# Kernel tuning notes

Hardware: AMD Instinct MI355X
Metric: run time of the kernel (lower is better)

## Reference

```python
import jax, jax.numpy as jnp
import numpy as np

N_NODES = 100000
N_EDGES = 1600000
IN_FEATS = 128
HIDDEN = 128
NUM_CLASSES = 4


def setup_inputs() -> dict:
    key = jax.random.key(0)
    ks = jax.random.split(key, 8)
    features = jax.random.normal(ks[0], (N_NODES, IN_FEATS), dtype=jnp.float32)
    src = jax.random.randint(ks[1], (N_EDGES,), 0, N_NODES, dtype=jnp.int64)
    dst = jax.random.randint(ks[2], (N_EDGES,), 0, N_NODES, dtype=jnp.int64)
    s = 1.0 / np.sqrt(IN_FEATS)
    W1 = jax.random.normal(ks[3], (IN_FEATS, HIDDEN), dtype=jnp.float32) * s
    b1 = jnp.zeros((HIDDEN,), dtype=jnp.float32)
    W2 = jax.random.normal(ks[4], (HIDDEN, HIDDEN), dtype=jnp.float32) * s
    b2 = jnp.zeros((HIDDEN,), dtype=jnp.float32)
    Wc = jax.random.normal(ks[5], (HIDDEN, NUM_CLASSES), dtype=jnp.float32) * s
    bc = jnp.zeros((NUM_CLASSES,), dtype=jnp.float32)
    return {"features": features, "src": src, "dst": dst,
            "W1": W1, "b1": b1, "W2": W2, "b2": b2, "Wc": Wc, "bc": bc}


def _graph_conv(x, W, b, src, dst, n_nodes, activation=True):
    # DGL GraphConv, norm='both': D_out^{-1/2} A^T D_in... i.e. symmetric norm.
    ones = jnp.ones((src.shape[0],), dtype=x.dtype)
    deg_out = jnp.clip(jax.ops.segment_sum(ones, src, num_segments=n_nodes), 1.0)
    deg_in = jnp.clip(jax.ops.segment_sum(ones, dst, num_segments=n_nodes), 1.0)
    # scale sources, project (in >= out so matmul first, math-equivalent), gather-scatter
    h = (x * (deg_out ** -0.5)[:, None]) @ W            # [N, out]
    msg = h[src]                                         # [E, out] gather
    agg = jax.ops.segment_sum(msg, dst, num_segments=n_nodes)  # [N, out] scatter-add
    h = agg * (deg_in ** -0.5)[:, None] + b
    return jax.nn.relu(h) if activation else h


def reference(features, src, dst, W1, b1, W2, b2, Wc, bc):
    # eval-mode forward: dropout is identity
    n = features.shape[0]
    h = _graph_conv(features, W1, b1, src, dst, n, activation=True)
    h = _graph_conv(h, W2, b2, src, dst, n, activation=True)
    return h @ Wc + bc  # [N, num_classes] logits
```

## Files before the change

kernel.cpp:

```cpp
#include <hip/hip_runtime.h>
#include <hip/hip_fp16.h>
#include <math.h>

#define N_NODES 100000
#define N_EDGES 1600000
#define F 128
#define NBUK 196
#define BSH 9
#define BSZ 512
#define CAP 10240
#define NPART 784

typedef _Float16 half8 __attribute__((ext_vector_type(8)));
typedef float    f32x4 __attribute__((ext_vector_type(4)));
typedef int      i32x4 __attribute__((ext_vector_type(4)));

__global__ __launch_bounds__(256) void init_pack(int* __restrict__ curD,
                                                 int* __restrict__ curS,
                                                 _Float16* __restrict__ padrow1,
                                                 _Float16* __restrict__ padrow2,
                                                 const float* __restrict__ W1,
                                                 const float* __restrict__ W2,
                                                 _Float16* __restrict__ hi1,
                                                 _Float16* __restrict__ lo1,
                                                 _Float16* __restrict__ hi2,
                                                 _Float16* __restrict__ lo2)
{
    int t = threadIdx.x;
    if (blockIdx.x == 0) {
        if (t < NBUK) { curD[t] = t * CAP; curS[t] = t * CAP; }
        if (t < 16) reinterpret_cast<int4*>(padrow1)[t] = make_int4(0, 0, 0, 0);
        else if (t >= 32 && t < 48) reinterpret_cast<int4*>(padrow2)[t - 32] = make_int4(0, 0, 0, 0);
        return;
    }
    int gidx = (blockIdx.x - 1) * 256 + t;
    const float* W = (gidx < 16384) ? W1 : W2;
    _Float16* hi = (gidx < 16384) ? hi1 : hi2;
    _Float16* lo = (gidx < 16384) ? lo1 : lo2;
    int idx = gidx & 16383;
    int f = idx >> 9, r = idx & 511;
    int l = r >> 3, j = r & 7;
    int kc = f >> 3, ct = f & 7;
    int k = kc * 32 + (l >> 4) * 8 + j;
    int n = ct * 16 + (l & 15);
    float w = W[k * 128 + n];
    _Float16 h = (_Float16)w;
    hi[idx] = h;
    lo[idx] = (_Float16)(w - (float)h);
}

__global__ __launch_bounds__(512) void part_gemm1(const int* __restrict__ src,
                                                  const int* __restrict__ dst,
                                                  int* __restrict__ curD,
                                                  int* __restrict__ curS,
                                                  int* __restrict__ bukD,
                                                  unsigned short* __restrict__ bukS,
                                                  const float* __restrict__ X,
                                                  const _Float16* __restrict__ Whi,
                                                  const _Float16* __restrict__ Wlo,
                                                  _Float16* __restrict__ Y, int N)
{
    __shared__ int hd[NBUK], hs[NBUK], bd[NBUK], bs[NBUK], cd[NBUK], cs[NBUK];
    const int tid = threadIdx.x;

    if (blockIdx.x < NPART) {
        const int chunk = (((N_EDGES + NPART - 1) / NPART) + 3) & ~3;
        const int beg = blockIdx.x * chunk;
        const int end = min(beg + chunk, N_EDGES);
        if (beg >= end) return;
        if (tid < NBUK) { hd[tid] = 0; hs[tid] = 0; cd[tid] = 0; cs[tid] = 0; }
        __syncthreads();
        const int b4 = beg >> 2, e4 = end >> 2;
        const int i0 = b4 + tid;
        const bool v0 = i0 < e4;
        i32x4 d0 = {}, s0 = {};
        if (v0) {
            d0 = reinterpret_cast<const i32x4*>(dst)[i0];
            s0 = reinterpret_cast<const i32x4*>(src)[i0];
            atomicAdd(&hd[d0.x >> BSH], 1); atomicAdd(&hd[d0.y >> BSH], 1);
            atomicAdd(&hd[d0.z >> BSH], 1); atomicAdd(&hd[d0.w >> BSH], 1);
            atomicAdd(&hs[s0.x >> BSH], 1); atomicAdd(&hs[s0.y >> BSH], 1);
            atomicAdd(&hs[s0.z >> BSH], 1); atomicAdd(&hs[s0.w >> BSH], 1);
        }
        __syncthreads();
        if (tid < NBUK) {
            bd[tid] = hd[tid] ? atomicAdd(&curD[tid], hd[tid]) : 0;
            bs[tid] = hs[tid] ? atomicAdd(&curS[tid], hs[tid]) : 0;
        }
        __syncthreads();
        if (v0) {
            int dd[4] = { d0.x, d0.y, d0.z, d0.w };
            int ss[4] = { s0.x, s0.y, s0.z, s0.w };
            #pragma unroll
            for (int j = 0; j < 4; j++) {
                int bin = dd[j] >> BSH;
                int r = atomicAdd(&cd[bin], 1);
                bukD[bd[bin] + r] = ((dd[j] & 511) << 17) | ss[j];
                int bin2 = ss[j] >> BSH;
                int r2 = atomicAdd(&cs[bin2], 1);
                bukS[bs[bin2] + r2] = (unsigned short)(ss[j] & 511);
            }
        }
        return;
    }

    const int l = tid & 63, w = tid >> 6;
    const int quad = l >> 4, m = l & 15;
    const int row0 = (blockIdx.x - NPART) * 256;
    const half8* Bh = reinterpret_cast<const half8*>(Whi);
    const half8* Bl = reinterpret_cast<const half8*>(Wlo);

    f32x4 acc[2][8] = {};

    for (int kc = 0; kc < 4; kc++) {
        half8 ah[2];
        #pragma unroll
        for (int rt = 0; rt < 2; rt++) {
            int grow = row0 + w * 32 + rt * 16 + m;
            float4 xa = make_float4(0.f, 0.f, 0.f, 0.f), xb = xa;
            if (grow < N) {
                const float4* Xp = reinterpret_cast<const float4*>(X) + (size_t)grow * 32 + kc * 8 + quad * 2;
                xa = Xp[0]; xb = Xp[1];
            }
            ah[rt][0] = (_Float16)xa.x; ah[rt][1] = (_Float16)xa.y;
            ah[rt][2] = (_Float16)xa.z; ah[rt][3] = (_Float16)xa.w;
            ah[rt][4] = (_Float16)xb.x; ah[rt][5] = (_Float16)xb.y;
            ah[rt][6] = (_Float16)xb.z; ah[rt][7] = (_Float16)xb.w;
        }
        #pragma unroll
        for (int ct = 0; ct < 8; ct++) {
            int f = kc * 8 + ct;
            half8 bh = Bh[f * 64 + l];
            half8 bl = Bl[f * 64 + l];
            #pragma unroll
            for (int rt = 0; rt < 2; rt++) {
                acc[rt][ct] = __builtin_amdgcn_mfma_f32_16x16x32_f16(ah[rt], bh, acc[rt][ct], 0, 0, 0);
                acc[rt][ct] = __builtin_amdgcn_mfma_f32_16x16x32_f16(ah[rt], bl, acc[rt][ct], 0, 0, 0);
            }
        }
    }

    #pragma unroll
    for (int rt = 0; rt < 2; rt++) {
        #pragma unroll
        for (int r = 0; r < 4; r++) {
            int grow = row0 + w * 32 + rt * 16 + quad * 4 + r;
            if (grow < N) {
                #pragma unroll
                for (int ct = 0; ct < 8; ct++)
                    Y[(size_t)grow * 128 + ct * 16 + m] = (_Float16)(acc[rt][ct][r]);
            }
        }
    }
}

__global__ __launch_bounds__(512) void deg_out(const unsigned short* __restrict__ bukS,
                                               const int* __restrict__ curS,
                                               float* __restrict__ sout)
{
    __shared__ int h[BSZ];
    const int tid = threadIdx.x;
    const int n0 = blockIdx.x << BSH;
    const int lo = blockIdx.x * CAP, hi = curS[blockIdx.x];
    const int cnt = hi - lo;
    h[tid] = 0;
    __syncthreads();
    const uint4* p8 = reinterpret_cast<const uint4*>(bukS + lo);
    const int nv = cnt >> 3;
    for (int j = tid; j < nv; j += 512) {
        uint4 v = p8[j];
        atomicAdd(&h[v.x & 0xFFFF], 1); atomicAdd(&h[v.x >> 16], 1);
        atomicAdd(&h[v.y & 0xFFFF], 1); atomicAdd(&h[v.y >> 16], 1);
        atomicAdd(&h[v.z & 0xFFFF], 1); atomicAdd(&h[v.z >> 16], 1);
        atomicAdd(&h[v.w & 0xFFFF], 1); atomicAdd(&h[v.w >> 16], 1);
    }
    for (int i = lo + (nv << 3) + tid; i < hi; i += 512)
        atomicAdd(&h[bukS[i]], 1);
    __syncthreads();
    int node = n0 + tid;
    if (node < N_NODES) sout[node] = rsqrtf((float)max(h[tid], 1));
}

__global__ __launch_bounds__(512) void csr_wv(const int* __restrict__ bukD,
                                              const int* __restrict__ curD,
                                              const float* __restrict__ sout,
                                              int* __restrict__ row_ptr,
                                              float* __restrict__ sin_,
                                              int* __restrict__ col,
                                              float* __restrict__ wv)
{
    __shared__ int h[BSZ], sc[BSZ], cur[BSZ];
    const int tid = threadIdx.x;
    const int n0 = blockIdx.x << BSH;
    const int lo = blockIdx.x * CAP, hi = curD[blockIdx.x];
    const int cnt = hi - lo;
    h[tid] = 0;
    __syncthreads();
    const i32x4* p4 = reinterpret_cast<const i32x4*>(bukD + lo);
    const int nv = cnt >> 2;
    for (int j = tid; j < nv; j += 512) {
        i32x4 v = p4[j];
        atomicAdd(&h[((unsigned)v.x) >> 17], 1);
        atomicAdd(&h[((unsigned)v.y) >> 17], 1);
        atomicAdd(&h[((unsigned)v.z) >> 17], 1);
        atomicAdd(&h[((unsigned)v.w) >> 17], 1);
    }
    for (int i = lo + (nv << 2) + tid; i < hi; i += 512)
        atomicAdd(&h[((unsigned)bukD[i]) >> 17], 1);
    __syncthreads();
    int own = h[tid];
    int own4 = (own + 3) & ~3;
    sc[tid] = own4;
    __syncthreads();
    for (int off = 1; off < 512; off <<= 1) {
        int u = (tid >= off) ? sc[tid - off] : 0;
        __syncthreads();
        sc[tid] += u;
        __syncthreads();
    }
    int ex = sc[tid] - own4;
    cur[tid] = ex;
    int node = n0 + tid;
    if (node < N_NODES) {
        row_ptr[2 * node]     = lo + ex;
        row_ptr[2 * node + 1] = lo + ex + own4;
        sin_[node] = rsqrtf((float)max(own, 1));
    }
    __syncthreads();
    for (int j = tid; j < nv; j += 512) {
        i32x4 v = p4[j];
        int pv[4] = { v.x, v.y, v.z, v.w };
        #pragma unroll
        for (int q = 0; q < 4; q++) {
            int p = pv[q];
            int s = p & 0x1FFFF;
            int r = atomicAdd(&cur[((unsigned)p) >> 17], 1);
            col[lo + r] = s;
            wv[lo + r]  = sout[s];
        }
    }
    for (int i = lo + (nv << 2) + tid; i < hi; i += 512) {
        int p = bukD[i];
        int s = p & 0x1FFFF;
        int r = atomicAdd(&cur[((unsigned)p) >> 17], 1);
        col[lo + r] = s;
        wv[lo + r]  = sout[s];
    }
    for (int k = own; k < own4; k++) {
        col[lo + ex + k] = N_NODES;
        wv[lo + ex + k]  = 0.f;
    }
}

#define ACCW(vv, ww) \
    a0 = fmaf(ww, (float)vv[0], a0); a1 = fmaf(ww, (float)vv[1], a1); \
    a2 = fmaf(ww, (float)vv[2], a2); a3 = fmaf(ww, (float)vv[3], a3); \
    a4 = fmaf(ww, (float)vv[4], a4); a5 = fmaf(ww, (float)vv[5], a5); \
    a6 = fmaf(ww, (float)vv[6], a6); a7 = fmaf(ww, (float)vv[7], a7);

#define ACCU(vv) \
    a0 += (float)vv[0]; a1 += (float)vv[1]; a2 += (float)vv[2]; a3 += (float)vv[3]; \
    a4 += (float)vv[4]; a5 += (float)vv[5]; a6 += (float)vv[6]; a7 += (float)vv[7];

__global__ __launch_bounds__(256) void gather_gemm2(const _Float16* __restrict__ Hh,
                                                    const int* __restrict__ row_ptr,
                                                    const int* __restrict__ col,
                                                    const float* __restrict__ wv,
                                                    const float* __restrict__ sin_,
                                                    const float* __restrict__ bias,
                                                    const _Float16* __restrict__ Whi,
                                                    const _Float16* __restrict__ Wlo,
                                                    const float* __restrict__ sout,
                                                    _Float16* __restrict__ Y)
{
    __shared__ _Float16 At[16][128];
    const int tid = threadIdx.x;
    const int sub  = tid & 15;
    const int g0   = tid >> 4;
    const int node = blockIdx.x * 16 + g0;
    const int beg = row_ptr[2 * node], end = row_ptr[2 * node + 1];
    const half8* __restrict__ H8 = reinterpret_cast<const half8*>(Hh);

    float a0 = 0.f, a1 = 0.f, a2 = 0.f, a3 = 0.f, a4 = 0.f, a5 = 0.f, a6 = 0.f, a7 = 0.f;
    int i = beg;
    for (; i + 8 <= end; i += 8) {
        int4 ca = *reinterpret_cast<const int4*>(col + i);
        int4 cb = *reinterpret_cast<const int4*>(col + i + 4);
        float4 wa = *reinterpret_cast<const float4*>(wv + i);
        float4 wb = *reinterpret_cast<const float4*>(wv + i + 4);
        half8 v0 = H8[((size_t)ca.x << 4) | sub];
        half8 v1 = H8[((size_t)ca.y << 4) | sub];
        half8 v2 = H8[((size_t)ca.z << 4) | sub];
        half8 v3 = H8[((size_t)ca.w << 4) | sub];
        half8 v4 = H8[((size_t)cb.x << 4) | sub];
        half8 v5 = H8[((size_t)cb.y << 4) | sub];
        half8 v6 = H8[((size_t)cb.z << 4) | sub];
        half8 v7 = H8[((size_t)cb.w << 4) | sub];
        ACCW(v0, wa.x) ACCW(v1, wa.y) ACCW(v2, wa.z) ACCW(v3, wa.w)
        ACCW(v4, wb.x) ACCW(v5, wb.y) ACCW(v6, wb.z) ACCW(v7, wb.w)
    }
    if (i < end) {
        int4 ca = *reinterpret_cast<const int4*>(col + i);
        float4 wa = *reinterpret_cast<const float4*>(wv + i);
        half8 v0 = H8[((size_t)ca.x << 4) | sub];
        half8 v1 = H8[((size_t)ca.y << 4) | sub];
        half8 v2 = H8[((size_t)ca.z << 4) | sub];
        half8 v3 = H8[((size_t)ca.w << 4) | sub];
        ACCW(v0, wa.x) ACCW(v1, wa.y) ACCW(v2, wa.z) ACCW(v3, wa.w)
    }
    {
        float scn = sin_[node];
        const float4* B4 = reinterpret_cast<const float4*>(bias);
        float4 bA = B4[2 * sub], bB = B4[2 * sub + 1];
        half8 o;
        o[0] = (_Float16)fmaxf(fmaf(a0, scn, bA.x), 0.f);
        o[1] = (_Float16)fmaxf(fmaf(a1, scn, bA.y), 0.f);
        o[2] = (_Float16)fmaxf(fmaf(a2, scn, bA.z), 0.f);
        o[3] = (_Float16)fmaxf(fmaf(a3, scn, bA.w), 0.f);
        o[4] = (_Float16)fmaxf(fmaf(a4, scn, bB.x), 0.f);
        o[5] = (_Float16)fmaxf(fmaf(a5, scn, bB.y), 0.f);
        o[6] = (_Float16)fmaxf(fmaf(a6, scn, bB.z), 0.f);
        o[7] = (_Float16)fmaxf(fmaf(a7, scn, bB.w), 0.f);
        int wc = sub ^ (g0 & 7);
        *reinterpret_cast<half8*>(&At[g0][wc * 8]) = o;
    }
    __syncthreads();

    const int l = tid & 63, w = tid >> 6;
    const int quad = l >> 4, m = l & 15;
    const half8* Bh = reinterpret_cast<const half8*>(Whi);
    const half8* Bl = reinterpret_cast<const half8*>(Wlo);

    f32x4 acc0 = {}, acc1 = {};
    #pragma unroll
    for (int kc = 0; kc < 4; kc++) {
        int rc = (kc * 4 + quad) ^ (m & 7);
        half8 a = *reinterpret_cast<const half8*>(&At[m][rc * 8]);
        int f0 = kc * 8 + w * 2;
        half8 bh0 = Bh[f0 * 64 + l];
        half8 bl0 = Bl[f0 * 64 + l];
        half8 bh1 = Bh[(f0 + 1) * 64 + l];
        half8 bl1 = Bl[(f0 + 1) * 64 + l];
        acc0 = __builtin_amdgcn_mfma_f32_16x16x32_f16(a, bh0, acc0, 0, 0, 0);
        acc0 = __builtin_amdgcn_mfma_f32_16x16x32_f16(a, bl0, acc0, 0, 0, 0);
        acc1 = __builtin_amdgcn_mfma_f32_16x16x32_f16(a, bh1, acc1, 0, 0, 0);
        acc1 = __builtin_amdgcn_mfma_f32_16x16x32_f16(a, bl1, acc1, 0, 0, 0);
    }

    const int rbase = blockIdx.x * 16 + quad * 4;
    const int c0 = (w * 2) * 16 + m;
    #pragma unroll
    for (int r = 0; r < 4; r++) {
        int grow = rbase + r;
        float s = sout[grow];
        Y[(size_t)grow * 128 + c0]      = (_Float16)(acc0[r] * s);
        Y[(size_t)grow * 128 + c0 + 16] = (_Float16)(acc1[r] * s);
    }
}

__global__ __launch_bounds__(256) void gather_cls(const _Float16* __restrict__ Hh,
                                                  const int* __restrict__ row_ptr,
                                                  const int* __restrict__ col,
                                                  const float* __restrict__ sin_,
                                                  const float* __restrict__ bias,
                                                  const float* __restrict__ Wc,
                                                  const float* __restrict__ bc,
                                                  float* __restrict__ out, int N)
{
    __shared__ float4 Wcs[128];
    for (int t = threadIdx.x; t < 128; t += 256)
        Wcs[t] = reinterpret_cast<const float4*>(Wc)[t];
    __syncthreads();

    const int sub  = threadIdx.x & 15;
    const int node = blockIdx.x * 16 + (threadIdx.x >> 4);
    if (node >= N) return;
    const int beg = row_ptr[2 * node], end = row_ptr[2 * node + 1];
    const half8* __restrict__ H8 = reinterpret_cast<const half8*>(Hh);

    float a0 = 0.f, a1 = 0.f, a2 = 0.f, a3 = 0.f, a4 = 0.f, a5 = 0.f, a6 = 0.f, a7 = 0.f;
    int i = beg;
    for (; i + 8 <= end; i += 8) {
        int4 ca = *reinterpret_cast<const int4*>(col + i);
        int4 cb = *reinterpret_cast<const int4*>(col + i + 4);
        half8 v0 = H8[((size_t)ca.x << 4) | sub];
        half8 v1 = H8[((size_t)ca.y << 4) | sub];
        half8 v2 = H8[((size_t)ca.z << 4) | sub];
        half8 v3 = H8[((size_t)ca.w << 4) | sub];
        half8 v4 = H8[((size_t)cb.x << 4) | sub];
        half8 v5 = H8[((size_t)cb.y << 4) | sub];
        half8 v6 = H8[((size_t)cb.z << 4) | sub];
        half8 v7 = H8[((size_t)cb.w << 4) | sub];
        ACCU(v0) ACCU(v1) ACCU(v2) ACCU(v3)
        ACCU(v4) ACCU(v5) ACCU(v6) ACCU(v7)
    }
    if (i < end) {
        int4 ca = *reinterpret_cast<const int4*>(col + i);
        half8 v0 = H8[((size_t)ca.x << 4) | sub];
        half8 v1 = H8[((size_t)ca.y << 4) | sub];
        half8 v2 = H8[((size_t)ca.z << 4) | sub];
        half8 v3 = H8[((size_t)ca.w << 4) | sub];
        ACCU(v0) ACCU(v1) ACCU(v2) ACCU(v3)
    }
    float scn = sin_[node];
    const float4* B4 = reinterpret_cast<const float4*>(bias);
    float4 bA = B4[2 * sub], bB = B4[2 * sub + 1];
    float h0 = fmaxf(fmaf(a0, scn, bA.x), 0.f);
    float h1 = fmaxf(fmaf(a1, scn, bA.y), 0.f);
    float h2 = fmaxf(fmaf(a2, scn, bA.z), 0.f);
    float h3 = fmaxf(fmaf(a3, scn, bA.w), 0.f);
    float h4 = fmaxf(fmaf(a4, scn, bB.x), 0.f);
    float h5 = fmaxf(fmaf(a5, scn, bB.y), 0.f);
    float h6 = fmaxf(fmaf(a6, scn, bB.z), 0.f);
    float h7 = fmaxf(fmaf(a7, scn, bB.w), 0.f);

    float lx = 0.f, ly = 0.f, lz = 0.f, lw = 0.f;
    float4 w;
    w = Wcs[sub * 8 + 0]; lx = fmaf(h0, w.x, lx); ly = fmaf(h0, w.y, ly); lz = fmaf(h0, w.z, lz); lw = fmaf(h0, w.w, lw);
    w = Wcs[sub * 8 + 1]; lx = fmaf(h1, w.x, lx); ly = fmaf(h1, w.y, ly); lz = fmaf(h1, w.z, lz); lw = fmaf(h1, w.w, lw);
    w = Wcs[sub * 8 + 2]; lx = fmaf(h2, w.x, lx); ly = fmaf(h2, w.y, ly); lz = fmaf(h2, w.z, lz); lw = fmaf(h2, w.w, lw);
    w = Wcs[sub * 8 + 3]; lx = fmaf(h3, w.x, lx); ly = fmaf(h3, w.y, ly); lz = fmaf(h3, w.z, lz); lw = fmaf(h3, w.w, lw);
    w = Wcs[sub * 8 + 4]; lx = fmaf(h4, w.x, lx); ly = fmaf(h4, w.y, ly); lz = fmaf(h4, w.z, lz); lw = fmaf(h4, w.w, lw);
    w = Wcs[sub * 8 + 5]; lx = fmaf(h5, w.x, lx); ly = fmaf(h5, w.y, ly); lz = fmaf(h5, w.z, lz); lw = fmaf(h5, w.w, lw);
    w = Wcs[sub * 8 + 6]; lx = fmaf(h6, w.x, lx); ly = fmaf(h6, w.y, ly); lz = fmaf(h6, w.z, lz); lw = fmaf(h6, w.w, lw);
    w = Wcs[sub * 8 + 7]; lx = fmaf(h7, w.x, lx); ly = fmaf(h7, w.y, ly); lz = fmaf(h7, w.z, lz); lw = fmaf(h7, w.w, lw);

    #pragma unroll
    for (int m = 1; m < 16; m <<= 1) {
        lx += __shfl_xor(lx, m);
        ly += __shfl_xor(ly, m);
        lz += __shfl_xor(lz, m);
        lw += __shfl_xor(lw, m);
    }
    if (sub == 0) {
        float4 bcv = reinterpret_cast<const float4*>(bc)[0];
        float4 r;
        r.x = lx + bcv.x; r.y = ly + bcv.y; r.z = lz + bcv.z; r.w = lw + bcv.w;
        reinterpret_cast<float4*>(out)[node] = r;
    }
}

extern "C" void kernel_launch(void* const* d_in, const int* in_sizes, int n_in,
                              void* d_out, int out_size, void* d_ws, size_t ws_size,
                              hipStream_t stream)
{
    const float* features = (const float*)d_in[0];
    const int*   src      = (const int*)d_in[1];
    const int*   dst      = (const int*)d_in[2];
    const float* W1       = (const float*)d_in[3];
    const float* b1       = (const float*)d_in[4];
    const float* W2       = (const float*)d_in[5];
    const float* b2       = (const float*)d_in[6];
    const float* Wc       = (const float*)d_in[7];
    const float* bc       = (const float*)d_in[8];
    float* out = (float*)d_out;

    char* ws = (char*)d_ws;
    const size_t MB = 1 << 20;
    int* curD  = (int*)(ws + 0);
    int* curS  = (int*)(ws + 1024);
    _Float16* Whi1 = (_Float16*)(ws + 64 * 1024);
    _Float16* Wlo1 = (_Float16*)(ws + 96 * 1024);
    _Float16* Whi2 = (_Float16*)(ws + 128 * 1024);
    _Float16* Wlo2 = (_Float16*)(ws + 160 * 1024);
    float* sout    = (float*)(ws + 512 * 1024);
    float* sin_    = (float*)(ws + 1 * MB);
    int*   row_ptr = (int*)(ws + 2 * MB);
    int*   col     = (int*)(ws + 3 * MB);
    float* wv      = (float*)(ws + 11 * MB);
    _Float16* hMsg = (_Float16*)(ws + 25 * MB);
    int*   bukD    = (int*)(ws + 52 * MB);
    unsigned short* bukS = (unsigned short*)(ws + 60 * MB);
    _Float16* hA   = (_Float16*)(ws + 52 * MB);

    const int N = N_NODES;
    const int NGB = (N + 15) / 16;

    init_pack<<<129, 256, 0, stream>>>(curD, curS,
                                       hMsg + (size_t)N * F, hA + (size_t)N * F,
                                       W1, W2, Whi1, Wlo1, Whi2, Wlo2);

    part_gemm1<<<NPART + 391, 512, 0, stream>>>(src, dst, curD, curS, bukD, bukS,
                                                features, Whi1, Wlo1, hMsg, N);

    deg_out<<<NBUK, 512, 0, stream>>>(bukS, curS, sout);

    csr_wv<<<NBUK, 512, 0, stream>>>(bukD, curD, sout, row_ptr, sin_, col, wv);

    gather_gemm2<<<NGB, 256, 0, stream>>>(hMsg, row_ptr, col, wv, sin_, b1,
                                          Whi2, Wlo2, sout, hA);

    gather_cls<<<NGB, 256, 0, stream>>>(hA, row_ptr, col, sin_, b2, Wc, bc, out, N);
}
```

Before: 294.6 us.

## Fold source-degree scaling into GEMM1 output and drop per-edge weight array

The out-degree normalization is now applied to each row of the first projection (which is moved after deg_out and co-launched with CSR construction) instead of being stored per edge in a wv array. The layer-1 gather then does plain unweighted sums, removing the per-edge weight reads and writes and the random sout lookups during CSR build. In exchange the GEMM now waits for the degree pass instead of overlapping with edge partitioning, and scaling happens before the fp16 rounding.

Result: faster. 285.1 us (median of 2 runs) (-3.2%).

```diff
diff --git a/kernel.cpp b/kernel.cpp
--- a/kernel.cpp
+++ b/kernel.cpp
@@ -49,64 +49,155 @@
     lo[idx] = (_Float16)(w - (float)h);
 }
 
-__global__ __launch_bounds__(512) void part_gemm1(const int* __restrict__ src,
+__global__ __launch_bounds__(512) void part_edges(const int* __restrict__ src,
                                                   const int* __restrict__ dst,
                                                   int* __restrict__ curD,
                                                   int* __restrict__ curS,
                                                   int* __restrict__ bukD,
-                                                  unsigned short* __restrict__ bukS,
-                                                  const float* __restrict__ X,
-                                                  const _Float16* __restrict__ Whi,
-                                                  const _Float16* __restrict__ Wlo,
-                                                  _Float16* __restrict__ Y, int N)
+                                                  unsigned short* __restrict__ bukS)
 {
     __shared__ int hd[NBUK], hs[NBUK], bd[NBUK], bs[NBUK], cd[NBUK], cs[NBUK];
     const int tid = threadIdx.x;
-
-    if (blockIdx.x < NPART) {
-        const int chunk = (((N_EDGES + NPART - 1) / NPART) + 3) & ~3;
-        const int beg = blockIdx.x * chunk;
-        const int end = min(beg + chunk, N_EDGES);
-        if (beg >= end) return;
-        if (tid < NBUK) { hd[tid] = 0; hs[tid] = 0; cd[tid] = 0; cs[tid] = 0; }
+    const int chunk = (((N_EDGES + NPART - 1) / NPART) + 3) & ~3;
+    const int beg = blockIdx.x * chunk;
+    const int end = min(beg + chunk, N_EDGES);
+    if (beg >= end) return;
+    if (tid < NBUK) { hd[tid] = 0; hs[tid] = 0; cd[tid] = 0; cs[tid] = 0; }
+    __syncthreads();
+    const int b4 = beg >> 2, e4 = end >> 2;
+    const int i0 = b4 + tid;
+    const bool v0 = i0 < e4;
+    i32x4 d0 = {}, s0 = {};
+    if (v0) {
+        d0 = reinterpret_cast<const i32x4*>(dst)[i0];
+        s0 = reinterpret_cast<const i32x4*>(src)[i0];
+        atomicAdd(&hd[d0.x >> BSH], 1); atomicAdd(&hd[d0.y >> BSH], 1);
+        atomicAdd(&hd[d0.z >> BSH], 1); atomicAdd(&hd[d0.w >> BSH], 1);
+        atomicAdd(&hs[s0.x >> BSH], 1); atomicAdd(&hs[s0.y >> BSH], 1);
+        atomicAdd(&hs[s0.z >> BSH], 1); atomicAdd(&hs[s0.w >> BSH], 1);
+    }
+    __syncthreads();
+    if (tid < NBUK) {
+        bd[tid] = hd[tid] ? atomicAdd(&curD[tid], hd[tid]) : 0;
+        bs[tid] = hs[tid] ? atomicAdd(&curS[tid], hs[tid]) : 0;
+    }
+    __syncthreads();
+    if (v0) {
+        int dd[4] = { d0.x, d0.y, d0.z, d0.w };
+        int ss[4] = { s0.x, s0.y, s0.z, s0.w };
+        #pragma unroll
+        for (int j = 0; j < 4; j++) {
+            int bin = dd[j] >> BSH;
+            int r = atomicAdd(&cd[bin], 1);
+            bukD[bd[bin] + r] = ((dd[j] & 511) << 17) | ss[j];
+            int bin2 = ss[j] >> BSH;
+            int r2 = atomicAdd(&cs[bin2], 1);
+            bukS[bs[bin2] + r2] = (unsigned short)(ss[j] & 511);
+        }
+    }
+}
+
+__global__ __launch_bounds__(512) void deg_out(const unsigned short* __restrict__ bukS,
+                                               const int* __restrict__ curS,
+                                               float* __restrict__ sout)
+{
+    __shared__ int h[BSZ];
+    const int tid = threadIdx.x;
+    const int n0 = blockIdx.x << BSH;
+    const int lo = blockIdx.x * CAP, hi = curS[blockIdx.x];
+    const int cnt = hi - lo;
+    h[tid] = 0;
+    __syncthreads();
+    const uint4* p8 = reinterpret_cast<const uint4*>(bukS + lo);
+    const int nv = cnt >> 3;
+    for (int j = tid; j < nv; j += 512) {
+        uint4 v = p8[j];
+        atomicAdd(&h[v.x & 0xFFFF], 1); atomicAdd(&h[v.x >> 16], 1);
+        atomicAdd(&h[v.y & 0xFFFF], 1); atomicAdd(&h[v.y >> 16], 1);
+        atomicAdd(&h[v.z & 0xFFFF], 1); atomicAdd(&h[v.z >> 16], 1);
+        atomicAdd(&h[v.w & 0xFFFF], 1); atomicAdd(&h[v.w >> 16], 1);
+    }
+    for (int i = lo + (nv << 3) + tid; i < hi; i += 512)
+        atomicAdd(&h[bukS[i]], 1);
+    __syncthreads();
+    int node = n0 + tid;
+    if (node < N_NODES) sout[node] = rsqrtf((float)max(h[tid], 1));
+}
+
+__global__ __launch_bounds__(512) void csr_gemm1(const int* __restrict__ bukD,
+                                                 const int* __restrict__ curD,
+                                                 int* __restrict__ row_ptr,
+                                                 float* __restrict__ sin_,
+                                                 int* __restrict__ col,
+                                                 const float* __restrict__ X,
+                                                 const _Float16* __restrict__ Whi,
+                                                 const _Float16* __restrict__ Wlo,
+                                                 const float* __restrict__ sout,
+                                                 _Float16* __restrict__ Y, int N)
+{
+    __shared__ int h[BSZ], sc[BSZ], cur[BSZ];
+    const int tid = threadIdx.x;
+
+    if (blockIdx.x < NBUK) {
+        const int n0 = blockIdx.x << BSH;
+        const int lo = blockIdx.x * CAP, hi = curD[blockIdx.x];
+        const int cnt = hi - lo;
+        h[tid] = 0;
         __syncthreads();
-        const int b4 = beg >> 2, e4 = end >> 2;
-        const int i0 = b4 + tid;
-        const bool v0 = i0 < e4;
-        i32x4 d0 = {}, s0 = {};
-        if (v0) {
-            d0 = reinterpret_cast<const i32x4*>(dst)[i0];
-            s0 = reinterpret_cast<const i32x4*>(src)[i0];
-            atomicAdd(&hd[d0.x >> BSH], 1); atomicAdd(&hd[d0.y >> BSH], 1);
-            atomicAdd(&hd[d0.z >> BSH], 1); atomicAdd(&hd[d0.w >> BSH], 1);
-            atomicAdd(&hs[s0.x >> BSH], 1); atomicAdd(&hs[s0.y >> BSH], 1);
-            atomicAdd(&hs[s0.z >> BSH], 1); atomicAdd(&hs[s0.w >> BSH], 1);
-        }
+        const i32x4* p4 = reinterpret_cast<const i32x4*>(bukD + lo);
+        const int nv = cnt >> 2;
+        for (int j = tid; j < nv; j += 512) {
+            i32x4 v = p4[j];
+            atomicAdd(&h[((unsigned)v.x) >> 17], 1);
+            atomicAdd(&h[((unsigned)v.y) >> 17], 1);
+            atomicAdd(&h[((unsigned)v.z) >> 17], 1);
+            atomicAdd(&h[((unsigned)v.w) >> 17], 1);
+        }
+        for (int i = lo + (nv << 2) + tid; i < hi; i += 512)
+            atomicAdd(&h[((unsigned)bukD[i]) >> 17], 1);
         __syncthreads();
-        if (tid < NBUK) {
-            bd[tid] = hd[tid] ? atomicAdd(&curD[tid], hd[tid]) : 0;
-            bs[tid] = hs[tid] ? atomicAdd(&curS[tid], hs[tid]) : 0;
-        }
+        int own = h[tid];
+        int own4 = (own + 3) & ~3;
+        sc[tid] = own4;
         __syncthreads();
-        if (v0) {
-            int dd[4] = { d0.x, d0.y, d0.z, d0.w };
-            int ss[4] = { s0.x, s0.y, s0.z, s0.w };
+        for (int off = 1; off < 512; off <<= 1) {
+            int u = (tid >= off) ? sc[tid - off] : 0;
+            __syncthreads();
+            sc[tid] += u;
+            __syncthreads();
+        }
+        int ex = sc[tid] - own4;
+        cur[tid] = ex;
+        int node = n0 + tid;
+        if (node < N_NODES) {
+            row_ptr[2 * node]     = lo + ex;
+            row_ptr[2 * node + 1] = lo + ex + own4;
+            sin_[node] = rsqrtf((float)max(own, 1));
+        }
+        __syncthreads();
+        for (int j = tid; j < nv; j += 512) {
+            i32x4 v = p4[j];
+            int pv[4] = { v.x, v.y, v.z, v.w };
             #pragma unroll
-            for (int j = 0; j < 4; j++) {
-                int bin = dd[j] >> BSH;
-                int r = atomicAdd(&cd[bin], 1);
-                bukD[bd[bin] + r] = ((dd[j] & 511) << 17) | ss[j];
-                int bin2 = ss[j] >> BSH;
-                int r2 = atomicAdd(&cs[bin2], 1);
-                bukS[bs[bin2] + r2] = (unsigned short)(ss[j] & 511);
+            for (int q = 0; q < 4; q++) {
+                int p = pv[q];
+                int r = atomicAdd(&cur[((unsigned)p) >> 17], 1);
+                col[lo + r] = p & 0x1FFFF;
             }
         }
+        for (int i = lo + (nv << 2) + tid; i < hi; i += 512) {
+            int p = bukD[i];
+            int r = atomicAdd(&cur[((unsigned)p) >> 17], 1);
+            col[lo + r] = p & 0x1FFFF;
+        }
+        for (int k = own; k < own4; k++)
+            col[lo + ex + k] = N_NODES;
         return;
     }
 
     const int l = tid & 63, w = tid >> 6;
     const int quad = l >> 4, m = l & 15;
-    const int row0 = (blockIdx.x - NPART) * 256;
+    const int row0 = (blockIdx.x - NBUK) * 256;
     const half8* Bh = reinterpret_cast<const half8*>(Whi);
     const half8* Bl = reinterpret_cast<const half8*>(Wlo);
 
@@ -146,117 +237,14 @@
         for (int r = 0; r < 4; r++) {
             int grow = row0 + w * 32 + rt * 16 + quad * 4 + r;
             if (grow < N) {
+                float s = sout[grow];
                 #pragma unroll
                 for (int ct = 0; ct < 8; ct++)
-                    Y[(size_t)grow * 128 + ct * 16 + m] = (_Float16)(acc[rt][ct][r]);
+                    Y[(size_t)grow * 128 + ct * 16 + m] = (_Float16)(acc[rt][ct][r] * s);
             }
         }
     }
 }
-
-__global__ __launch_bounds__(512) void deg_out(const unsigned short* __restrict__ bukS,
-                                               const int* __restrict__ curS,
-                                               float* __restrict__ sout)
-{
-    __shared__ int h[BSZ];
-    const int tid = threadIdx.x;
-    const int n0 = blockIdx.x << BSH;
-    const int lo = blockIdx.x * CAP, hi = curS[blockIdx.x];
-    const int cnt = hi - lo;
-    h[tid] = 0;
-    __syncthreads();
-    const uint4* p8 = reinterpret_cast<const uint4*>(bukS + lo);
-    const int nv = cnt >> 3;
-    for (int j = tid; j < nv; j += 512) {
-        uint4 v = p8[j];
-        atomicAdd(&h[v.x & 0xFFFF], 1); atomicAdd(&h[v.x >> 16], 1);
-        atomicAdd(&h[v.y & 0xFFFF], 1); atomicAdd(&h[v.y >> 16], 1);
-        atomicAdd(&h[v.z & 0xFFFF], 1); atomicAdd(&h[v.z >> 16], 1);
-        atomicAdd(&h[v.w & 0xFFFF], 1); atomicAdd(&h[v.w >> 16], 1);
-    }
-    for (int i = lo + (nv << 3) + tid; i < hi; i += 512)
-        atomicAdd(&h[bukS[i]], 1);
-    __syncthreads();
-    int node = n0 + tid;
-    if (node < N_NODES) sout[node] = rsqrtf((float)max(h[tid], 1));
-}
-
-__global__ __launch_bounds__(512) void csr_wv(const int* __restrict__ bukD,
-                                              const int* __restrict__ curD,
-                                              const float* __restrict__ sout,
-                                              int* __restrict__ row_ptr,
-                                              float* __restrict__ sin_,
-                                              int* __restrict__ col,
-                                              float* __restrict__ wv)
-{
-    __shared__ int h[BSZ], sc[BSZ], cur[BSZ];
-    const int tid = threadIdx.x;
-    const int n0 = blockIdx.x << BSH;
-    const int lo = blockIdx.x * CAP, hi = curD[blockIdx.x];
-    const int cnt = hi - lo;
-    h[tid] = 0;
-    __syncthreads();
-    const i32x4* p4 = reinterpret_cast<const i32x4*>(bukD + lo);
-    const int nv = cnt >> 2;
-    for (int j = tid; j < nv; j += 512) {
-        i32x4 v = p4[j];
-        atomicAdd(&h[((unsigned)v.x) >> 17], 1);
-        atomicAdd(&h[((unsigned)v.y) >> 17], 1);
-        atomicAdd(&h[((unsigned)v.z) >> 17], 1);
-        atomicAdd(&h[((unsigned)v.w) >> 17], 1);
-    }
-    for (int i = lo + (nv << 2) + tid; i < hi; i += 512)
-        atomicAdd(&h[((unsigned)bukD[i]) >> 17], 1);
-    __syncthreads();
-    int own = h[tid];
-    int own4 = (own + 3) & ~3;
-    sc[tid] = own4;
-    __syncthreads();
-    for (int off = 1; off < 512; off <<= 1) {
-        int u = (tid >= off) ? sc[tid - off] : 0;
-        __syncthreads();
-        sc[tid] += u;
-        __syncthreads();
-    }
-    int ex = sc[tid] - own4;
-    cur[tid] = ex;
-    int node = n0 + tid;
-    if (node < N_NODES) {
-        row_ptr[2 * node]     = lo + ex;
-        row_ptr[2 * node + 1] = lo + ex + own4;
-        sin_[node] = rsqrtf((float)max(own, 1));
-    }
-    __syncthreads();
-    for (int j = tid; j < nv; j += 512) {
-        i32x4 v = p4[j];
-        int pv[4] = { v.x, v.y, v.z, v.w };
-        #pragma unroll
-        for (int q = 0; q < 4; q++) {
-            int p = pv[q];
-            int s = p & 0x1FFFF;
-            int r = atomicAdd(&cur[((unsigned)p) >> 17], 1);
-            col[lo + r] = s;
-            wv[lo + r]  = sout[s];
-        }
-    }
-    for (int i = lo + (nv << 2) + tid; i < hi; i += 512) {
-        int p = bukD[i];
-        int s = p & 0x1FFFF;
-        int r = atomicAdd(&cur[((unsigned)p) >> 17], 1);
-        col[lo + r] = s;
-        wv[lo + r]  = sout[s];
-    }
-    for (int k = own; k < own4; k++) {
-        col[lo + ex + k] = N_NODES;
-        wv[lo + ex + k]  = 0.f;
-    }
-}
-
-#define ACCW(vv, ww) \
-    a0 = fmaf(ww, (float)vv[0], a0); a1 = fmaf(ww, (float)vv[1], a1); \
-    a2 = fmaf(ww, (float)vv[2], a2); a3 = fmaf(ww, (float)vv[3], a3); \
-    a4 = fmaf(ww, (float)vv[4], a4); a5 = fmaf(ww, (float)vv[5], a5); \
-    a6 = fmaf(ww, (float)vv[6], a6); a7 = fmaf(ww, (float)vv[7], a7);
 
 #define ACCU(vv) \
     a0 += (float)vv[0]; a1 += (float)vv[1]; a2 += (float)vv[2]; a3 += (float)vv[3]; \
@@ -265,7 +253,6 @@
 __global__ __launch_bounds__(256) void gather_gemm2(const _Float16* __restrict__ Hh,
                                                     const int* __restrict__ row_ptr,
                                                     const int* __restrict__ col,
-                                                    const float* __restrict__ wv,
                                                     const float* __restrict__ sin_,
                                                     const float* __restrict__ bias,
                                                     const _Float16* __restrict__ Whi,
@@ -286,8 +273,6 @@
     for (; i + 8 <= end; i += 8) {
         int4 ca = *reinterpret_cast<const int4*>(col + i);
         int4 cb = *reinterpret_cast<const int4*>(col + i + 4);
-        float4 wa = *reinterpret_cast<const float4*>(wv + i);
-        float4 wb = *reinterpret_cast<const float4*>(wv + i + 4);
         half8 v0 = H8[((size_t)ca.x << 4) | sub];
         half8 v1 = H8[((size_t)ca.y << 4) | sub];
         half8 v2 = H8[((size_t)ca.z << 4) | sub];
@@ -296,17 +281,16 @@
         half8 v5 = H8[((size_t)cb.y << 4) | sub];
         half8 v6 = H8[((size_t)cb.z << 4) | sub];
         half8 v7 = H8[((size_t)cb.w << 4) | sub];
-        ACCW(v0, wa.x) ACCW(v1, wa.y) ACCW(v2, wa.z) ACCW(v3, wa.w)
-        ACCW(v4, wb.x) ACCW(v5, wb.y) ACCW(v6, wb.z) ACCW(v7, wb.w)
+        ACCU(v0) ACCU(v1) ACCU(v2) ACCU(v3)
+        ACCU(v4) ACCU(v5) ACCU(v6) ACCU(v7)
     }
     if (i < end) {
         int4 ca = *reinterpret_cast<const int4*>(col + i);
-        float4 wa = *reinterpret_cast<const float4*>(wv + i);
         half8 v0 = H8[((size_t)ca.x << 4) | sub];
         half8 v1 = H8[((size_t)ca.y << 4) | sub];
         half8 v2 = H8[((size_t)ca.z << 4) | sub];
         half8 v3 = H8[((size_t)ca.w << 4) | sub];
-        ACCW(v0, wa.x) ACCW(v1, wa.y) ACCW(v2, wa.z) ACCW(v3, wa.w)
+        ACCU(v0) ACCU(v1) ACCU(v2) ACCU(v3)
     }
     {
         float scn = sin_[node];
@@ -467,7 +451,6 @@
     float* sin_    = (float*)(ws + 1 * MB);
     int*   row_ptr = (int*)(ws + 2 * MB);
     int*   col     = (int*)(ws + 3 * MB);
-    float* wv      = (float*)(ws + 11 * MB);
     _Float16* hMsg = (_Float16*)(ws + 25 * MB);
     int*   bukD    = (int*)(ws + 52 * MB);
     unsigned short* bukS = (unsigned short*)(ws + 60 * MB);
@@ -480,14 +463,14 @@
                                        hMsg + (size_t)N * F, hA + (size_t)N * F,
                                        W1, W2, Whi1, Wlo1, Whi2, Wlo2);
 
-    part_gemm1<<<NPART + 391, 512, 0, stream>>>(src, dst, curD, curS, bukD, bukS,
-                                                features, Whi1, Wlo1, hMsg, N);
+    part_edges<<<NPART, 512, 0, stream>>>(src, dst, curD, curS, bukD, bukS);
 
     deg_out<<<NBUK, 512, 0, stream>>>(bukS, curS, sout);
 
-    csr_wv<<<NBUK, 512, 0, stream>>>(bukD, curD, sout, row_ptr, sin_, col, wv);
-
-    gather_gemm2<<<NGB, 256, 0, stream>>>(hMsg, row_ptr, col, wv, sin_, b1,
+    csr_gemm1<<<NBUK + 391, 512, 0, stream>>>(bukD, curD, row_ptr, sin_, col,
+                                              features, Whi1, Wlo1, sout, hMsg, N);
+
+    gather_gemm2<<<NGB, 256, 0, stream>>>(hMsg, row_ptr, col, sin_, b1,
                                           Whi2, Wlo2, sout, hA);
 
     gather_cls<<<NGB, 256, 0, stream>>>(hA, row_ptr, col, sin_, b2, Wc, bc, out, N);
```
